# Kernel tuning notes

Hardware: AMD Instinct MI355X
Metric: run time of the kernel (lower is better)

The kernel has to match this reference:

```python
import jax, jax.numpy as jnp
import numpy as np

D_MODEL = 1024


def setup_inputs() -> dict:
    key = jax.random.key(0)
    ks = jax.random.split(key, 7)
    B, S, D = 4, 2048, D_MODEL
    scale = 1.0 / np.sqrt(D)
    inp = {
        "query": jax.random.normal(ks[0], (B, S, D), dtype=jnp.float32),
        "key": jax.random.normal(ks[1], (B, S, D), dtype=jnp.float32),
        "value": jax.random.normal(ks[2], (B, S, D), dtype=jnp.float32),
        # NOTE: original torch code applies query_projection to q, k AND v,
        # so only one projection weight (Wq) participates, plus output proj.
        "Wq": (jax.random.normal(ks[3], (D, D), dtype=jnp.float32) * scale),
        "bq": jnp.zeros((D,), dtype=jnp.float32),
        "Wo": (jax.random.normal(ks[4], (D, D), dtype=jnp.float32) * scale),
        "bo": jnp.zeros((D,), dtype=jnp.float32),
    }
    return inp


def reference(query, key, value, Wq, bq, Wo, bo):
    # Faithful to source: same projection (Wq, bq) used for q, k, v.
    q = jnp.einsum("bsd,de->bse", query, Wq) + bq   # (B, S, D)
    k = jnp.einsum("btd,de->bte", key, Wq) + bq     # (B, T, D)
    v = jnp.einsum("btd,de->bte", value, Wq) + bq   # (B, T, D)
    # No 1/sqrt(d) scaling in the original.
    score = jnp.einsum("bse,bte->bst", q, k)        # (B, S, T)
    weights = jax.nn.softmax(score, axis=-1)
    # Dropout is identity in eval / for a deterministic reference.
    ctx = jnp.einsum("bst,bte->bse", weights, v)    # (B, S, D)
    out = jnp.einsum("bse,ef->bsf", ctx, Wo) + bo   # (B, S, D)
    return (out, weights)
```

## Files before the change

### kernel.cpp

```cpp
#include <hip/hip_runtime.h>

typedef unsigned short u16;
typedef unsigned int u32;
typedef signed char i8;
typedef __bf16 bf16x8 __attribute__((ext_vector_type(8)));
typedef float f32x4 __attribute__((ext_vector_type(4)));
typedef int i32x4 __attribute__((ext_vector_type(4)));
typedef i8 i8x4 __attribute__((ext_vector_type(4)));
typedef u16 u16x8 __attribute__((ext_vector_type(8)));

#define AS1(p) ((const __attribute__((address_space(1))) void*)(p))
#define AS3(p) ((__attribute__((address_space(3))) void*)(p))

__device__ __forceinline__ u16 f2bf(float x) {
  u32 u = __float_as_uint(x);
  u32 r = u + 0x7fffu + ((u >> 16) & 1u);
  return (u16)(r >> 16);
}
__device__ __forceinline__ float bf2f(u16 h) {
  return __uint_as_float(((u32)h) << 16);
}

#define S_IN (8.0f / 127.0f)
#define S_W (0.25f / 127.0f)
#define S_QK (8.0f / 127.0f)
#define INV_S_IN (127.0f / 8.0f)
#define INV_S_W (508.0f)
#define INV_S_QK (127.0f / 8.0f)

__device__ __forceinline__ int2 q8i(float x, float inv_s) {
  float t = fminf(fmaxf(x * inv_s, -126.99f), 126.99f);
  float hf = rintf(t);
  float lf = fminf(fmaxf(rintf((t - hf) * 256.0f), -127.0f), 127.0f);
  return make_int2((int)hf, (int)lf);
}

__global__ __launch_bounds__(256) void prep_all(
    const float* __restrict__ q, const float* __restrict__ k,
    const float* __restrict__ value, const float* __restrict__ Wq,
    const float* __restrict__ Wo, i8* __restrict__ qh, i8* __restrict__ ql,
    i8* __restrict__ kh, i8* __restrict__ kl, u16* __restrict__ valT,
    i8* __restrict__ wqt_h, i8* __restrict__ wqt_l, u16* __restrict__ wot,
    u16* __restrict__ wq_b) {
  __shared__ float tileA[32][33];
  __shared__ float tileB[32][33];
  const int bid = blockIdx.x;
  const int tid = threadIdx.x;
  const int D = 1024;

  if (bid < 8192) {
    const int bx = bid & 31;
    const int by = (bid >> 5) & 63;
    const int bz = bid >> 11;
    const int tx = tid & 31, ty = tid >> 5;
    const int c0 = bx * 32, r0 = by * 32;
    const size_t zi = (size_t)bz * 2048 * 1024;
#pragma unroll
    for (int i = ty; i < 32; i += 8)
      tileA[i][tx] = value[zi + (size_t)(r0 + i) * D + (c0 + tx)];
    __syncthreads();
#pragma unroll
    for (int i = ty; i < 32; i += 8)
      valT[zi + (size_t)(c0 + i) * 2048 + (r0 + tx)] = f2bf(tileA[tx][i]);
  } else if (bid < 10240) {
    const int b2 = bid - 8192;
    const int n4 = 2097152;
    const int stride = 2048 * 256;
    for (int i = b2 * 256 + tid; i < n4; i += stride) {
      float4 x = ((const float4*)q)[i];
      float xs[4] = {x.x, x.y, x.z, x.w};
      i8x4 h, l;
#pragma unroll
      for (int e = 0; e < 4; ++e) {
        int2 r = q8i(xs[e], INV_S_IN);
        h[e] = (i8)r.x;
        l[e] = (i8)r.y;
      }
      ((i8x4*)qh)[i] = h;
      ((i8x4*)ql)[i] = l;
      x = ((const float4*)k)[i];
      float ys[4] = {x.x, x.y, x.z, x.w};
#pragma unroll
      for (int e = 0; e < 4; ++e) {
        int2 r = q8i(ys[e], INV_S_IN);
        h[e] = (i8)r.x;
        l[e] = (i8)r.y;
      }
      ((i8x4*)kh)[i] = h;
      ((i8x4*)kl)[i] = l;
    }
  } else {
    const int r = bid - 10240;
    const int bx = r & 31, by = r >> 5;
    const int tx = tid & 31, ty = tid >> 5;
    const int c0 = bx * 32, r0 = by * 32;
#pragma unroll
    for (int i = ty; i < 32; i += 8) {
      float xq = Wq[(size_t)(r0 + i) * D + c0 + tx];
      tileA[i][tx] = xq;
      wq_b[(size_t)(r0 + i) * D + c0 + tx] = f2bf(xq);
      tileB[i][tx] = Wo[(size_t)(r0 + i) * D + c0 + tx];
    }
    __syncthreads();
#pragma unroll
    for (int i = ty; i < 32; i += 8) {
      float x = tileA[tx][i];
      int2 rr = q8i(x, INV_S_W);
      size_t o = (size_t)(c0 + i) * D + r0 + tx;
      wqt_h[o] = (i8)rr.x;
      wqt_l[o] = (i8)rr.y;
      wot[o] = f2bf(tileB[tx][i]);
    }
  }
}

__global__ __launch_bounds__(256) void bqo_kernel(const float* __restrict__ bq,
                                                  const u16* __restrict__ wot,
                                                  const float* __restrict__ bo,
                                                  float* __restrict__ bqo,
                                                  int D) {
  const int f = blockIdx.x * 4 + (threadIdx.x >> 6);
  const int lane = threadIdx.x & 63;
  const u16* wr_ = wot + (size_t)f * D;
  float s = 0.f;
  for (int e = lane; e < D; e += 64) s += bq[e] * bf2f(wr_[e]);
#pragma unroll
  for (int off = 32; off; off >>= 1) s += __shfl_xor(s, off);
  if (lane == 0) bqo[f] = s + bo[f];
}

template <int EPI>
__global__ __launch_bounds__(256, 2) void gemm_bt(
    const u16* __restrict__ Ah, const u16* __restrict__ Bh,
    const float* __restrict__ bias, float* __restrict__ Cf,
    u16* __restrict__ Ch, int M, int N, int K,
    long long sA, long long sB, long long sC) {
  __shared__ alignas(16) u16 As[128 * 32];
  __shared__ alignas(16) u16 Bs[128 * 32];

  const int t = threadIdx.x;
  const int lane = t & 63;
  const int w = t >> 6;
  const int wr = w >> 1, wc = w & 1;

  const long long zb = blockIdx.z;
  const u16* pA = Ah + zb * sA;
  const u16* pB = Bh + zb * sB;

  const int m0 = blockIdx.x * 128;
  const int n0 = blockIdx.y * 128;

  f32x4 acc[4][4] = {};

  const int row0 = t >> 2;
  const int colS = (t & 3) * 8;
  const int lds0 = (t & ~63) * 8;
  const int lds1 = (256 + (t & ~63)) * 8;

  const size_t aoff0 = (size_t)(m0 + row0) * K + colS;
  const size_t aoff1 = (size_t)(m0 + row0 + 64) * K + colS;
  const size_t boff0 = (size_t)(n0 + row0) * K + colS;
  const size_t boff1 = (size_t)(n0 + row0 + 64) * K + colS;

  for (int k0 = 0; k0 < K; k0 += 32) {
    __syncthreads();
    __builtin_amdgcn_global_load_lds(AS1(pA + aoff0 + k0), AS3(&As[lds0]), 16, 0, 0);
    __builtin_amdgcn_global_load_lds(AS1(pA + aoff1 + k0), AS3(&As[lds1]), 16, 0, 0);
    __builtin_amdgcn_global_load_lds(AS1(pB + boff0 + k0), AS3(&Bs[lds0]), 16, 0, 0);
    __builtin_amdgcn_global_load_lds(AS1(pB + boff1 + k0), AS3(&Bs[lds1]), 16, 0, 0);
    __syncthreads();

    const int fr = lane & 15;
    const int kc = (lane >> 4) * 8;
    bf16x8 a[4], b[4];
#pragma unroll
    for (int i = 0; i < 4; ++i)
      a[i] = *(const bf16x8*)&As[(wr * 64 + i * 16 + fr) * 32 + kc];
#pragma unroll
    for (int j = 0; j < 4; ++j)
      b[j] = *(const bf16x8*)&Bs[(wc * 64 + j * 16 + fr) * 32 + kc];
#pragma unroll
    for (int i = 0; i < 4; ++i)
#pragma unroll
      for (int j = 0; j < 4; ++j)
        acc[i][j] = __builtin_amdgcn_mfma_f32_16x16x32_bf16(a[i], b[j], acc[i][j], 0, 0, 0);
  }

  const int er = (lane >> 4) * 4;
  const int ec = lane & 15;
#pragma unroll
  for (int j = 0; j < 4; ++j) {
    const int gcol = n0 + wc * 64 + j * 16 + ec;
    const float bv = bias ? bias[gcol] : 0.0f;
#pragma unroll
    for (int i = 0; i < 4; ++i) {
      const int grow0 = m0 + wr * 64 + i * 16 + er;
#pragma unroll
      for (int r = 0; r < 4; ++r) {
        const float x = acc[i][j][r] + bv;
        const size_t off = (size_t)zb * sC + (size_t)(grow0 + r) * N + gcol;
        if constexpr (EPI == 0) Cf[off] = x;
        else Ch[off] = f2bf(x);
      }
    }
  }
}

#define STG_I(DSTBASE, SH, SL, ROWBASE, KREAL)                                 \
  do {                                                                         \
    const i8* s0_ = (sc < 4 ? (SH) : (SL)) +                                   \
                    (size_t)((ROWBASE) + sr) * K + (KREAL) + ((sc & 3) << 4);  \
    const i8* s1_ = s0_ + (size_t)64 * K;                                      \
    __builtin_amdgcn_global_load_lds(AS1(s0_), AS3(&lds8[(DSTBASE) + ldsB]), 16, 0, 0); \
    __builtin_amdgcn_global_load_lds(AS1(s1_), AS3(&lds8[(DSTBASE) + 8192 + ldsB]), 16, 0, 0); \
  } while (0)

#define LDA_IV(BUF)                                                            \
  do {                                                                         \
    const int base_ = (BUF) * 49152;                                           \
    _Pragma("unroll") for (int i_ = 0; i_ < 4; ++i_) {                         \
      const int r_ = wr * 64 + i_ * 16 + fr;                                   \
      ah[i_] = *(const i32x4*)&lds8[base_ + r_ * 128 + ((ksl ^ (r_ & 7)) << 4)]; \
      al[i_] = *(const i32x4*)&lds8[base_ + r_ * 128 + (((4 + ksl) ^ (r_ & 7)) << 4)]; \
    }                                                                          \
  } while (0)

#define LDB_IV(BUF)                                                            \
  do {                                                                         \
    const int base_ = (BUF) * 49152 + 32768;                                   \
    _Pragma("unroll") for (int j_ = 0; j_ < 4; ++j_) {                         \
      const int r_ = wc * 64 + j_ * 16 + fr;                                   \
      bh[j_] = *(const i32x4*)&lds8[base_ + r_ * 128 + ((ksl ^ (r_ & 7)) << 4)]; \
      bl[j_] = *(const i32x4*)&lds8[base_ + r_ * 128 + (((4 + ksl) ^ (r_ & 7)) << 4)]; \
    }                                                                          \
  } while (0)

#define MMA_IV()                                                               \
  do {                                                                         \
    _Pragma("unroll") for (int j_ = 0; j_ < 4; ++j_) {                         \
      _Pragma("unroll") for (int i_ = 0; i_ < 4; ++i_) {                       \
        accH[i_][j_] = __builtin_amdgcn_mfma_i32_16x16x64_i8(                  \
            ah[i_], bh[j_], accH[i_][j_], 0, 0, 0);                            \
        accX[i_][j_] = __builtin_amdgcn_mfma_i32_16x16x64_i8(                  \
            ah[i_], bl[j_], accX[i_][j_], 0, 0, 0);                            \
        accX[i_][j_] = __builtin_amdgcn_mfma_i32_16x16x64_i8(                  \
            al[i_], bh[j_], accX[i_][j_], 0, 0, 0);                            \
      }                                                                        \
    }                                                                          \
  } while (0)

template <int EPI>
__global__ __launch_bounds__(512, 2) void gemm8i(
    const i8* __restrict__ Ah, const i8* __restrict__ Al,
    const i8* __restrict__ Bh, const i8* __restrict__ Bl,
    const float* __restrict__ bias, float sAB, float* __restrict__ Cf,
    i8* __restrict__ Ch, i8* __restrict__ Cl, int M, int N, int K,
    long long sA, long long sB, long long sC) {
  extern __shared__ i8 lds8[];

  const int tt = threadIdx.x;
  const int lane = tt & 63;
  const int wv = tt >> 6;
  const int wr = wv >> 1;
  const int wc = wv & 1;
  const int fr = lane & 15;
  const int ksl = lane >> 4;

  const long long zb = blockIdx.z;
  const i8* pAh = Ah + zb * sA;
  const i8* pAl = Al + zb * sA;
  const i8* pBh = Bh + zb * sB;
  const i8* pBl = Bl + zb * sB;
  const int m0 = blockIdx.x * 256;
  const int n0 = blockIdx.y * 128;

  const int sr = tt >> 3;
  const int ss = tt & 7;
  const int sc = ss ^ (sr & 7);
  const int ldsB = (tt & ~63) * 16;

  i32x4 accH[4][4] = {};
  i32x4 accX[4][4] = {};
  i32x4 ah[4], al[4], bh[4], bl[4];

  const int NT = K / 64;
  const int NITER = NT / 2;

  STG_I(0, pAh, pAl, m0, 0);
  STG_I(16384, pAh, pAl, m0 + 128, 0);
  STG_I(32768, pBh, pBl, n0, 0);
  STG_I(49152, pAh, pAl, m0, 64);
  STG_I(49152 + 16384, pAh, pAl, m0 + 128, 64);
  STG_I(49152 + 32768, pBh, pBl, n0, 64);
  asm volatile("s_waitcnt vmcnt(6)" ::: "memory");
  __builtin_amdgcn_s_barrier();

  for (int it = 0; it < NITER; ++it) {
    const int t0 = 2 * it;
    const int k2 = (t0 + 2 < NT ? t0 + 2 : NT - 1) * 64;
    const int k3 = (t0 + 3 < NT ? t0 + 3 : NT - 1) * 64;

    LDA_IV(0);
    LDB_IV(0);
    MMA_IV();
    asm volatile("s_waitcnt lgkmcnt(0)" ::: "memory");
    __builtin_amdgcn_s_barrier();
    STG_I(0, pAh, pAl, m0, k2);
    STG_I(16384, pAh, pAl, m0 + 128, k2);
    STG_I(32768, pBh, pBl, n0, k2);
    asm volatile("s_waitcnt vmcnt(6)" ::: "memory");
    __builtin_amdgcn_s_barrier();

    LDA_IV(1);
    LDB_IV(1);
    MMA_IV();
    asm volatile("s_waitcnt lgkmcnt(0)" ::: "memory");
    __builtin_amdgcn_s_barrier();
    STG_I(49152, pAh, pAl, m0, k3);
    STG_I(49152 + 16384, pAh, pAl, m0 + 128, k3);
    STG_I(49152 + 32768, pBh, pBl, n0, k3);
    asm volatile("s_waitcnt vmcnt(6)" ::: "memory");
    __builtin_amdgcn_s_barrier();
  }

  const int er = (lane >> 4) * 4;
  const int ec = lane & 15;
#pragma unroll
  for (int i = 0; i < 4; ++i) {
    const int grow0 = m0 + wr * 64 + i * 16 + er;
#pragma unroll
    for (int j = 0; j < 4; ++j) {
      const int gcol = n0 + wc * 64 + j * 16 + ec;
      const float bv = bias ? bias[gcol] : 0.0f;
#pragma unroll
      for (int r = 0; r < 4; ++r) {
        const float x =
            sAB * ((float)accH[i][j][r] + (float)accX[i][j][r] * 0.00390625f) + bv;
        const size_t off = (size_t)zb * sC + (size_t)(grow0 + r) * N + gcol;
        if constexpr (EPI == 0) {
          Cf[off] = x;
        } else {
          int2 qq = q8i(x, INV_S_QK);
          Ch[off] = (i8)qq.x;
          Cl[off] = (i8)qq.y;
        }
      }
    }
  }
}

#define STG_P(DSTBASE, SRC, ROWBASE, KREAL)                                    \
  do {                                                                         \
    const u16* s0_ = (SRC) + (size_t)((ROWBASE) + sr) * K + (KREAL) + (sc << 3); \
    const u16* s1_ = s0_ + (size_t)64 * K;                                     \
    __builtin_amdgcn_global_load_lds(AS1(s0_), AS3(&lds[(DSTBASE) + ldsW]), 16, 0, 0); \
    __builtin_amdgcn_global_load_lds(AS1(s1_), AS3(&lds[(DSTBASE) + 4096 + ldsW]), 16, 0, 0); \
  } while (0)

#define LDA_P(BUF, S, DST)                                                     \
  do {                                                                         \
    const int base_ = (BUF) * 24576;                                           \
    _Pragma("unroll") for (int i_ = 0; i_ < 4; ++i_) {                         \
      const int r_ = wr * 64 + i_ * 16 + fr;                                   \
      DST[i_] = *(const bf16x8*)&lds[base_ + r_ * 64 + (((((S) * 4 + ksl)) ^ (r_ & 7)) << 3)]; \
    }                                                                          \
  } while (0)

#define LDB_P(BUF, S, DST)                                                     \
  do {                                                                         \
    const int base_ = (BUF) * 24576 + 16384;                                   \
    _Pragma("unroll") for (int j_ = 0; j_ < 4; ++j_) {                         \
      const int r_ = wc * 64 + j_ * 16 + fr;                                   \
      DST[j_] = *(const bf16x8*)&lds[base_ + r_ * 64 + (((((S) * 4 + ksl)) ^ (r_ & 7)) << 3)]; \
    }                                                                          \
  } while (0)

#define MMA_P(A_, B_)                                                          \
  do {                                                                         \
    _Pragma("unroll") for (int i_ = 0; i_ < 4; ++i_) {                         \
      _Pragma("unroll") for (int j_ = 0; j_ < 4; ++j_) {                       \
        acc[i_][j_] = __builtin_amdgcn_mfma_f32_16x16x32_bf16(                 \
            A_[i_], B_[j_], acc[i_][j_], 0, 0, 0);                             \
      }                                                                        \
    }                                                                          \
  } while (0)

template <int EPI>
__global__ __launch_bounds__(512, 2) void gemm8p(
    const u16* __restrict__ A, const u16* __restrict__ B,
    const float* __restrict__ bias, float* __restrict__ Cf,
    u16* __restrict__ Ch, int M, int N, int K,
    long long sA, long long sB, long long sC) {
  extern __shared__ u16 lds[];

  const int tt = threadIdx.x;
  const int lane = tt & 63;
  const int wv = tt >> 6;
  const int wr = wv >> 1;
  const int wc = wv & 1;
  const int fr = lane & 15;
  const int ksl = lane >> 4;

  const long long zb = blockIdx.z;
  const u16* pA = A + zb * sA;
  const u16* pB = B + zb * sB;
  const int m0 = blockIdx.x * 256;
  const int n0 = blockIdx.y * 128;

  const int sr = tt >> 3;
  const int ss = tt & 7;
  const int sc = ss ^ (sr & 7);
  const int ldsW = (tt & ~63) * 8;

  f32x4 acc[4][4] = {};
  bf16x8 a0[4], a1[4], b0[4], b1[4];

  const int NT = K / 64;

  STG_P(16384, pB, n0, 0);
  STG_P(0, pA, m0, 0);
  STG_P(8192, pA, m0 + 128, 0);
  STG_P(24576 + 16384, pB, n0, 64);
  STG_P(24576 + 0, pA, m0, 64);
  STG_P(24576 + 8192, pA, m0 + 128, 64);
  asm volatile("s_waitcnt vmcnt(6)" ::: "memory");
  __builtin_amdgcn_s_barrier();

  for (int it = 0; it < NT; ++it) {
    const int cur = it & 1;
    const int nb = cur * 24576;
    const int kf = (it + 2 < NT ? it + 2 : NT - 1) * 64;

    LDA_P(cur, 0, a0);
    LDB_P(cur, 0, b0);
    LDA_P(cur, 1, a1);
    LDB_P(cur, 1, b1);
    MMA_P(a0, b0);
    MMA_P(a1, b1);
    asm volatile("s_waitcnt lgkmcnt(0)" ::: "memory");
    __builtin_amdgcn_s_barrier();
    STG_P(nb + 16384, pB, n0, kf);
    STG_P(nb + 0, pA, m0, kf);
    STG_P(nb + 8192, pA, m0 + 128, kf);
    asm volatile("s_waitcnt vmcnt(6)" ::: "memory");
    __builtin_amdgcn_s_barrier();
  }

  const int er = (lane >> 4) * 4;
  const int ec = lane & 15;
#pragma unroll
  for (int i = 0; i < 4; ++i) {
    const int grow0 = m0 + wr * 64 + i * 16 + er;
#pragma unroll
    for (int j = 0; j < 4; ++j) {
      const int gcol = n0 + wc * 64 + j * 16 + ec;
      const float bv = bias ? bias[gcol] : 0.0f;
#pragma unroll
      for (int r = 0; r < 4; ++r) {
        const float x = acc[i][j][r] + bv;
        const size_t off = (size_t)zb * sC + (size_t)(grow0 + r) * N + gcol;
        if constexpr (EPI == 0) Cf[off] = x;
        else Ch[off] = f2bf(x);
      }
    }
  }
}

__global__ __launch_bounds__(256) void softmax_rows_v(float* __restrict__ S,
                                                      u16* __restrict__ P) {
  const int T = 2048;
  const size_t row = blockIdx.x;
  float* sr = S + row * T;
  u16* prow = P + row * T;
  const int t = threadIdx.x;
  const int w = t >> 6, lane = t & 63;
  __shared__ float red[8];

  float4 r0 = ((const float4*)(sr + t * 8))[0];
  float4 r1 = ((const float4*)(sr + t * 8))[1];
  float v[8] = {r0.x, r0.y, r0.z, r0.w, r1.x, r1.y, r1.z, r1.w};
  float mx = -1e30f;
#pragma unroll
  for (int i = 0; i < 8; ++i) mx = fmaxf(mx, v[i]);
#pragma unroll
  for (int off = 32; off; off >>= 1) mx = fmaxf(mx, __shfl_xor(mx, off));
  if (lane == 0) red[w] = mx;
  __syncthreads();
  mx = fmaxf(fmaxf(red[0], red[1]), fmaxf(red[2], red[3]));

  float s = 0.f;
#pragma unroll
  for (int i = 0; i < 8; ++i) {
    v[i] = __expf(v[i] - mx);
    s += v[i];
  }
#pragma unroll
  for (int off = 32; off; off >>= 1) s += __shfl_xor(s, off);
  if (lane == 0) red[4 + w] = s;
  __syncthreads();
  s = (red[4] + red[5]) + (red[6] + red[7]);
  const float inv = 1.0f / s;

  u16x8 pv;
#pragma unroll
  for (int i = 0; i < 8; ++i) {
    v[i] *= inv;
    pv[i] = f2bf(v[i]);
  }
  float4* wr4 = (float4*)(sr + t * 8);
  wr4[0] = make_float4(v[0], v[1], v[2], v[3]);
  wr4[1] = make_float4(v[4], v[5], v[6], v[7]);
  ((u16x8*)prow)[t] = pv;
}

extern "C" void kernel_launch(void* const* d_in, const int* in_sizes, int n_in,
                              void* d_out, int out_size, void* d_ws,
                              size_t ws_size, hipStream_t stream) {
  (void)in_sizes; (void)n_in; (void)out_size; (void)ws_size;
  const float* query = (const float*)d_in[0];
  const float* key   = (const float*)d_in[1];
  const float* value = (const float*)d_in[2];
  const float* Wq    = (const float*)d_in[3];
  const float* bq    = (const float*)d_in[4];
  const float* Wo    = (const float*)d_in[5];
  const float* bo    = (const float*)d_in[6];

  const int S = 2048, D = 1024;
  const size_t n = (size_t)4 * S * D;

  float* out = (float*)d_out;
  float* wts = out + n;

  char* ws = (char*)d_ws;
  i8* wqt_h = (i8*)(ws);
  i8* wqt_l = (i8*)(ws + (1ull << 20));
  u16* wot  = (u16*)(ws + (2ull << 20));
  u16* wq_b = (u16*)(ws + (4ull << 20));
  u16* wqoT = (u16*)(ws + (6ull << 20));
  float* bqo = (float*)(ws + (8ull << 20));
  i8* QKh = (i8*)(ws + (9ull << 20));
  i8* QKl = (i8*)(ws + (25ull << 20));
  u16* tmp = (u16*)(ws + (41ull << 20));
  u16* P = (u16*)(ws + (9ull << 20));

  i8* ah = (i8*)wts;
  i8* al = ah + 2 * n;
  u16* valT = (u16*)out;

  hipFuncSetAttribute((const void*)&gemm8i<2>,
                      hipFuncAttributeMaxDynamicSharedMemorySize, 98304);
  hipFuncSetAttribute((const void*)&gemm8i<0>,
                      hipFuncAttributeMaxDynamicSharedMemorySize, 98304);
  hipFuncSetAttribute((const void*)&gemm8p<1>,
                      hipFuncAttributeMaxDynamicSharedMemorySize, 98304);
  hipFuncSetAttribute((const void*)&gemm8p<0>,
                      hipFuncAttributeMaxDynamicSharedMemorySize, 98304);

  prep_all<<<11264, 256, 0, stream>>>(query, key, value, Wq, Wo, ah, al,
                                      ah + n, al + n, valT, wqt_h, wqt_l, wot,
                                      wq_b);
  gemm_bt<1><<<dim3(8, 8, 1), 256, 0, stream>>>(
      wot, wq_b, nullptr, nullptr, wqoT, 1024, 1024, 1024, 0, 0, 0);
  bqo_kernel<<<256, 256, 0, stream>>>(bq, wot, bo, bqo, D);
  gemm8i<2><<<dim3(64, 8, 1), 512, 98304, stream>>>(
      ah, al, wqt_h, wqt_l, bq, S_IN * S_W, nullptr, QKh, QKl,
      16384, 1024, 1024, 0, 0, 0);
  gemm8i<0><<<dim3(8, 16, 4), 512, 98304, stream>>>(
      QKh, QKl, QKh + n, QKl + n, nullptr, S_QK * S_QK, wts, nullptr, nullptr,
      2048, 2048, 1024, (long long)S * D, (long long)S * D, (long long)S * S);
  softmax_rows_v<<<8192, 256, 0, stream>>>(wts, P);
  gemm8p<1><<<dim3(8, 8, 4), 512, 98304, stream>>>(
      P, valT, nullptr, nullptr, tmp, 2048, 1024, 2048, (long long)S * S,
      (long long)D * S, (long long)S * D);
  gemm8p<0><<<dim3(32, 8, 1), 512, 98304, stream>>>(
      tmp, wqoT, bqo, out, nullptr, 8192, 1024, 1024, 0, 0, 0);
}
```

Baseline: 272.4 us.

## Shrink int8 and bf16 GEMM tiles to 128x128 with 256-thread blocks

Both the split-int8 and bf16 GEMM kernels move from 256x128 tiles with 512 threads (8 waves) to 128x128 tiles with 256 threads (4 waves). Staging loads are restructured into four row-strided loads per thread, LDS per block drops from 96KB to 64KB, and launch grids double. This aims to raise occupancy and improve wave balance across CUs, at the cost of lower per-block operand reuse and more global and L2 traffic per FLOP.

```diff
diff --git a/kernel.cpp b/kernel.cpp
--- a/kernel.cpp
+++ b/kernel.cpp
@@ -206,18 +206,20 @@
   }
 }
 
-#define STG_I(DSTBASE, SH, SL, ROWBASE, KREAL)                                 \
-  do {                                                                         \
-    const i8* s0_ = (sc < 4 ? (SH) : (SL)) +                                   \
-                    (size_t)((ROWBASE) + sr) * K + (KREAL) + ((sc & 3) << 4);  \
-    const i8* s1_ = s0_ + (size_t)64 * K;                                      \
-    __builtin_amdgcn_global_load_lds(AS1(s0_), AS3(&lds8[(DSTBASE) + ldsB]), 16, 0, 0); \
-    __builtin_amdgcn_global_load_lds(AS1(s1_), AS3(&lds8[(DSTBASE) + 8192 + ldsB]), 16, 0, 0); \
-  } while (0)
-
-#define LDA_IV(BUF)                                                            \
-  do {                                                                         \
-    const int base_ = (BUF) * 49152;                                           \
+#define STG4_I(DSTBASE, SH, SL, ROWBASE, KREAL)                                \
+  do {                                                                         \
+    _Pragma("unroll") for (int p_ = 0; p_ < 4; ++p_) {                         \
+      const i8* s_ = (sc < 4 ? (SH) : (SL)) +                                  \
+                     (size_t)((ROWBASE) + p_ * 32 + sr) * K + (KREAL) +        \
+                     ((sc & 3) << 4);                                          \
+      __builtin_amdgcn_global_load_lds(                                        \
+          AS1(s_), AS3(&lds8[(DSTBASE) + p_ * 4096 + ldsB]), 16, 0, 0);        \
+    }                                                                          \
+  } while (0)
+
+#define LDA_I5(BUF)                                                            \
+  do {                                                                         \
+    const int base_ = (BUF) * 32768;                                           \
     _Pragma("unroll") for (int i_ = 0; i_ < 4; ++i_) {                         \
       const int r_ = wr * 64 + i_ * 16 + fr;                                   \
       ah[i_] = *(const i32x4*)&lds8[base_ + r_ * 128 + ((ksl ^ (r_ & 7)) << 4)]; \
@@ -225,9 +227,9 @@
     }                                                                          \
   } while (0)
 
-#define LDB_IV(BUF)                                                            \
-  do {                                                                         \
-    const int base_ = (BUF) * 49152 + 32768;                                   \
+#define LDB_I5(BUF)                                                            \
+  do {                                                                         \
+    const int base_ = (BUF) * 32768 + 16384;                                   \
     _Pragma("unroll") for (int j_ = 0; j_ < 4; ++j_) {                         \
       const int r_ = wc * 64 + j_ * 16 + fr;                                   \
       bh[j_] = *(const i32x4*)&lds8[base_ + r_ * 128 + ((ksl ^ (r_ & 7)) << 4)]; \
@@ -235,7 +237,7 @@
     }                                                                          \
   } while (0)
 
-#define MMA_IV()                                                               \
+#define MMA_I5()                                                               \
   do {                                                                         \
     _Pragma("unroll") for (int j_ = 0; j_ < 4; ++j_) {                         \
       _Pragma("unroll") for (int i_ = 0; i_ < 4; ++i_) {                       \
@@ -250,7 +252,7 @@
   } while (0)
 
 template <int EPI>
-__global__ __launch_bounds__(512, 2) void gemm8i(
+__global__ __launch_bounds__(256, 2) void gemm8i(
     const i8* __restrict__ Ah, const i8* __restrict__ Al,
     const i8* __restrict__ Bh, const i8* __restrict__ Bl,
     const float* __restrict__ bias, float sAB, float* __restrict__ Cf,
@@ -271,12 +273,11 @@
   const i8* pAl = Al + zb * sA;
   const i8* pBh = Bh + zb * sB;
   const i8* pBl = Bl + zb * sB;
-  const int m0 = blockIdx.x * 256;
+  const int m0 = blockIdx.x * 128;
   const int n0 = blockIdx.y * 128;
 
   const int sr = tt >> 3;
-  const int ss = tt & 7;
-  const int sc = ss ^ (sr & 7);
+  const int sc = (tt & 7) ^ (sr & 7);
   const int ldsB = (tt & ~63) * 16;
 
   i32x4 accH[4][4] = {};
@@ -284,42 +285,27 @@
   i32x4 ah[4], al[4], bh[4], bl[4];
 
   const int NT = K / 64;
-  const int NITER = NT / 2;
-
-  STG_I(0, pAh, pAl, m0, 0);
-  STG_I(16384, pAh, pAl, m0 + 128, 0);
-  STG_I(32768, pBh, pBl, n0, 0);
-  STG_I(49152, pAh, pAl, m0, 64);
-  STG_I(49152 + 16384, pAh, pAl, m0 + 128, 64);
-  STG_I(49152 + 32768, pBh, pBl, n0, 64);
-  asm volatile("s_waitcnt vmcnt(6)" ::: "memory");
+
+  STG4_I(0, pAh, pAl, m0, 0);
+  STG4_I(16384, pBh, pBl, n0, 0);
+  STG4_I(32768, pAh, pAl, m0, 64);
+  STG4_I(32768 + 16384, pBh, pBl, n0, 64);
+  asm volatile("s_waitcnt vmcnt(8)" ::: "memory");
   __builtin_amdgcn_s_barrier();
 
-  for (int it = 0; it < NITER; ++it) {
-    const int t0 = 2 * it;
-    const int k2 = (t0 + 2 < NT ? t0 + 2 : NT - 1) * 64;
-    const int k3 = (t0 + 3 < NT ? t0 + 3 : NT - 1) * 64;
-
-    LDA_IV(0);
-    LDB_IV(0);
-    MMA_IV();
+  for (int it = 0; it < NT; ++it) {
+    const int cur = it & 1;
+    const int nb = cur * 32768;
+    const int kf = (it + 2 < NT ? it + 2 : NT - 1) * 64;
+
+    LDA_I5(cur);
+    LDB_I5(cur);
+    MMA_I5();
     asm volatile("s_waitcnt lgkmcnt(0)" ::: "memory");
     __builtin_amdgcn_s_barrier();
-    STG_I(0, pAh, pAl, m0, k2);
-    STG_I(16384, pAh, pAl, m0 + 128, k2);
-    STG_I(32768, pBh, pBl, n0, k2);
-    asm volatile("s_waitcnt vmcnt(6)" ::: "memory");
-    __builtin_amdgcn_s_barrier();
-
-    LDA_IV(1);
-    LDB_IV(1);
-    MMA_IV();
-    asm volatile("s_waitcnt lgkmcnt(0)" ::: "memory");
-    __builtin_amdgcn_s_barrier();
-    STG_I(49152, pAh, pAl, m0, k3);
-    STG_I(49152 + 16384, pAh, pAl, m0 + 128, k3);
-    STG_I(49152 + 32768, pBh, pBl, n0, k3);
-    asm volatile("s_waitcnt vmcnt(6)" ::: "memory");
+    STG4_I(nb, pAh, pAl, m0, kf);
+    STG4_I(nb + 16384, pBh, pBl, n0, kf);
+    asm volatile("s_waitcnt vmcnt(8)" ::: "memory");
     __builtin_amdgcn_s_barrier();
   }
 
@@ -349,33 +335,35 @@
   }
 }
 
-#define STG_P(DSTBASE, SRC, ROWBASE, KREAL)                                    \
-  do {                                                                         \
-    const u16* s0_ = (SRC) + (size_t)((ROWBASE) + sr) * K + (KREAL) + (sc << 3); \
-    const u16* s1_ = s0_ + (size_t)64 * K;                                     \
-    __builtin_amdgcn_global_load_lds(AS1(s0_), AS3(&lds[(DSTBASE) + ldsW]), 16, 0, 0); \
-    __builtin_amdgcn_global_load_lds(AS1(s1_), AS3(&lds[(DSTBASE) + 4096 + ldsW]), 16, 0, 0); \
-  } while (0)
-
-#define LDA_P(BUF, S, DST)                                                     \
-  do {                                                                         \
-    const int base_ = (BUF) * 24576;                                           \
+#define STG4_P(DSTBASE, SRC, ROWBASE, KREAL)                                   \
+  do {                                                                         \
+    _Pragma("unroll") for (int p_ = 0; p_ < 4; ++p_) {                         \
+      const u16* s_ = (SRC) + (size_t)((ROWBASE) + p_ * 32 + sr) * K +         \
+                      (KREAL) + (sc << 3);                                     \
+      __builtin_amdgcn_global_load_lds(                                        \
+          AS1(s_), AS3(&lds[(DSTBASE) + p_ * 2048 + ldsW]), 16, 0, 0);         \
+    }                                                                          \
+  } while (0)
+
+#define LDA_P5(BUF, S, DST)                                                    \
+  do {                                                                         \
+    const int base_ = (BUF) * 16384;                                           \
     _Pragma("unroll") for (int i_ = 0; i_ < 4; ++i_) {                         \
       const int r_ = wr * 64 + i_ * 16 + fr;                                   \
       DST[i_] = *(const bf16x8*)&lds[base_ + r_ * 64 + (((((S) * 4 + ksl)) ^ (r_ & 7)) << 3)]; \
     }                                                                          \
   } while (0)
 
-#define LDB_P(BUF, S, DST)                                                     \
-  do {                                                                         \
-    const int base_ = (BUF) * 24576 + 16384;                                   \
+#define LDB_P5(BUF, S, DST)                                                    \
+  do {                                                                         \
+    const int base_ = (BUF) * 16384 + 8192;                                    \
     _Pragma("unroll") for (int j_ = 0; j_ < 4; ++j_) {                         \
       const int r_ = wc * 64 + j_ * 16 + fr;                                   \
       DST[j_] = *(const bf16x8*)&lds[base_ + r_ * 64 + (((((S) * 4 + ksl)) ^ (r_ & 7)) << 3)]; \
     }                                                                          \
   } while (0)
 
-#define MMA_P(A_, B_)                                                          \
+#define MMA_P5(A_, B_)                                                         \
   do {                                                                         \
     _Pragma("unroll") for (int i_ = 0; i_ < 4; ++i_) {                         \
       _Pragma("unroll") for (int j_ = 0; j_ < 4; ++j_) {                       \
@@ -386,7 +374,7 @@
   } while (0)
 
 template <int EPI>
-__global__ __launch_bounds__(512, 2) void gemm8p(
+__global__ __launch_bounds__(256, 2) void gemm8p(
     const u16* __restrict__ A, const u16* __restrict__ B,
     const float* __restrict__ bias, float* __restrict__ Cf,
     u16* __restrict__ Ch, int M, int N, int K,
@@ -404,12 +392,11 @@
   const long long zb = blockIdx.z;
   const u16* pA = A + zb * sA;
   const u16* pB = B + zb * sB;
-  const int m0 = blockIdx.x * 256;
+  const int m0 = blockIdx.x * 128;
   const int n0 = blockIdx.y * 128;
 
   const int sr = tt >> 3;
-  const int ss = tt & 7;
-  const int sc = ss ^ (sr & 7);
+  const int sc = (tt & 7) ^ (sr & 7);
   const int ldsW = (tt & ~63) * 8;
 
   f32x4 acc[4][4] = {};
@@ -417,32 +404,29 @@
 
   const int NT = K / 64;
 
-  STG_P(16384, pB, n0, 0);
-  STG_P(0, pA, m0, 0);
-  STG_P(8192, pA, m0 + 128, 0);
-  STG_P(24576 + 16384, pB, n0, 64);
-  STG_P(24576 + 0, pA, m0, 64);
-  STG_P(24576 + 8192, pA, m0 + 128, 64);
-  asm volatile("s_waitcnt vmcnt(6)" ::: "memory");
+  STG4_P(0, pA, m0, 0);
+  STG4_P(8192, pB, n0, 0);
+  STG4_P(16384, pA, m0, 64);
+  STG4_P(16384 + 8192, pB, n0, 64);
+  asm volatile("s_waitcnt vmcnt(8)" ::: "memory");
   __builtin_amdgcn_s_barrier();
 
   for (int it = 0; it < NT; ++it) {
     const int cur = it & 1;
-    const int nb = cur * 24576;
+    const int nb = cur * 16384;
     const int kf = (it + 2 < NT ? it + 2 : NT - 1) * 64;
 
-    LDA_P(cur, 0, a0);
-    LDB_P(cur, 0, b0);
-    LDA_P(cur, 1, a1);
-    LDB_P(cur, 1, b1);
-    MMA_P(a0, b0);
-    MMA_P(a1, b1);
+    LDA_P5(cur, 0, a0);
+    LDB_P5(cur, 0, b0);
+    LDA_P5(cur, 1, a1);
+    LDB_P5(cur, 1, b1);
+    MMA_P5(a0, b0);
+    MMA_P5(a1, b1);
     asm volatile("s_waitcnt lgkmcnt(0)" ::: "memory");
     __builtin_amdgcn_s_barrier();
-    STG_P(nb + 16384, pB, n0, kf);
-    STG_P(nb + 0, pA, m0, kf);
-    STG_P(nb + 8192, pA, m0 + 128, kf);
-    asm volatile("s_waitcnt vmcnt(6)" ::: "memory");
+    STG4_P(nb, pA, m0, kf);
+    STG4_P(nb + 8192, pB, n0, kf);
+    asm volatile("s_waitcnt vmcnt(8)" ::: "memory");
     __builtin_amdgcn_s_barrier();
   }
 
@@ -548,13 +532,13 @@
   u16* valT = (u16*)out;
 
   hipFuncSetAttribute((const void*)&gemm8i<2>,
-                      hipFuncAttributeMaxDynamicSharedMemorySize, 98304);
+                      hipFuncAttributeMaxDynamicSharedMemorySize, 65536);
   hipFuncSetAttribute((const void*)&gemm8i<0>,
-                      hipFuncAttributeMaxDynamicSharedMemorySize, 98304);
+                      hipFuncAttributeMaxDynamicSharedMemorySize, 65536);
   hipFuncSetAttribute((const void*)&gemm8p<1>,
-                      hipFuncAttributeMaxDynamicSharedMemorySize, 98304);
+                      hipFuncAttributeMaxDynamicSharedMemorySize, 65536);
   hipFuncSetAttribute((const void*)&gemm8p<0>,
-                      hipFuncAttributeMaxDynamicSharedMemorySize, 98304);
+                      hipFuncAttributeMaxDynamicSharedMemorySize, 65536);
 
   prep_all<<<11264, 256, 0, stream>>>(query, key, value, Wq, Wo, ah, al,
                                       ah + n, al + n, valT, wqt_h, wqt_l, wot,
@@ -562,16 +546,16 @@
   gemm_bt<1><<<dim3(8, 8, 1), 256, 0, stream>>>(
       wot, wq_b, nullptr, nullptr, wqoT, 1024, 1024, 1024, 0, 0, 0);
   bqo_kernel<<<256, 256, 0, stream>>>(bq, wot, bo, bqo, D);
-  gemm8i<2><<<dim3(64, 8, 1), 512, 98304, stream>>>(
+  gemm8i<2><<<dim3(128, 8, 1), 256, 65536, stream>>>(
       ah, al, wqt_h, wqt_l, bq, S_IN * S_W, nullptr, QKh, QKl,
       16384, 1024, 1024, 0, 0, 0);
-  gemm8i<0><<<dim3(8, 16, 4), 512, 98304, stream>>>(
+  gemm8i<0><<<dim3(16, 16, 4), 256, 65536, stream>>>(
       QKh, QKl, QKh + n, QKl + n, nullptr, S_QK * S_QK, wts, nullptr, nullptr,
       2048, 2048, 1024, (long long)S * D, (long long)S * D, (long long)S * S);
   softmax_rows_v<<<8192, 256, 0, stream>>>(wts, P);
-  gemm8p<1><<<dim3(8, 8, 4), 512, 98304, stream>>>(
+  gemm8p<1><<<dim3(16, 8, 4), 256, 65536, stream>>>(
       P, valT, nullptr, nullptr, tmp, 2048, 1024, 2048, (long long)S * S,
       (long long)D * S, (long long)S * D);
-  gemm8p<0><<<dim3(32, 8, 1), 512, 98304, stream>>>(
+  gemm8p<0><<<dim3(64, 8, 1), 256, 65536, stream>>>(
       tmp, wqoT, bqo, out, nullptr, 8192, 1024, 1024, 0, 0, 0);
 }
```

New measurement: 268.0 us. No clear change (-1.6%).
